# Optimization experiments

Measured on AMD Instinct MI355X. Metric: run time of the kernel, lower is better.

## Reference

```python
import jax, jax.numpy as jnp
import numpy as np

N, T, SAMPLES, OUT = 128, 1024, 1024, 8
TWO_PI = 2.0 * np.pi


def setup_inputs() -> dict:
    key = jax.random.key(0)
    ks = jax.random.split(key, 7)
    inp = jax.random.normal(ks[0], (N, T, 3), dtype=jnp.float32)
    h1, h2 = SAMPLES // 2, SAMPLES // 8
    W1 = jax.random.normal(ks[1], (h1, SAMPLES), dtype=jnp.float32) / np.sqrt(SAMPLES)
    b1 = jax.random.normal(ks[2], (h1,), dtype=jnp.float32) * 0.01
    W2 = jax.random.normal(ks[3], (h2, h1), dtype=jnp.float32) / np.sqrt(h1)
    b2 = jax.random.normal(ks[4], (h2,), dtype=jnp.float32) * 0.01
    W3 = jax.random.normal(ks[5], (OUT, h2), dtype=jnp.float32) / np.sqrt(h2)
    b3 = jax.random.normal(ks[6], (OUT,), dtype=jnp.float32) * 0.01
    return {"inp": inp, "W1": W1, "b1": b1, "W2": W2, "b2": b2, "W3": W3, "b3": b3}


def reference(inp, W1, b1, W2, b2, W3, b3):
    samples = W1.shape[1]
    t_len = inp.shape[1]
    x = inp[:, :, 0]          # [N, T] real signal
    day = inp[:, :, 2]        # [N, T] non-uniform times
    freqs = jnp.linspace(0.0, float(t_len - 1), samples, dtype=jnp.float32)
    # phase[n, s, t] = -2*pi * f_s * day[n, t]
    phase = (-TWO_PI) * freqs[None, :, None] * day[:, None, :]
    # complex exp split into real/imag panes; bmm fourier @ x -> [N, S]
    re = jnp.einsum('nst,nt->ns', jnp.cos(phase), x)
    im = jnp.einsum('nst,nt->ns', jnp.sin(phase), x)
    frequential = jnp.sqrt(re * re + im * im)  # |F x|, [N, samples]
    # 3-layer MLP with sigmoid activations (dropout = identity in eval)
    h = jax.nn.sigmoid(frequential @ W1.T + b1)
    h = jax.nn.sigmoid(h @ W2.T + b2)
    return h @ W3.T + b3
```

## Files before the change

kernel.cpp:

```cpp
#include <hip/hip_runtime.h>
#include <math.h>


#define NN   128
#define TT   1024
#define SS   1024
#define H1D  512
#define H2D  128
#define OUTD 8
#define KQN  8

#define MR    2048
#define WHALF 5
#define ALPHA 0.3702402f
#define BETA  6.35556e-6f
#define DSCALE 0.3432943f

#define OFF_SUBT 0
#define OFF_P1   (NN*512*4*2)

__device__ __forceinline__ float cos_rev(float r) { return __builtin_amdgcn_cosf(r); }
__device__ __forceinline__ float sin_rev(float r) { return __builtin_amdgcn_sinf(r); }

__device__ __forceinline__ float wave_sum(float v) {
#pragma unroll
    for (int off = 32; off > 0; off >>= 1) v += __shfl_xor(v, off, 64);
    return v;
}

__global__ __launch_bounds__(256) void k_sf(const float* __restrict__ inp,
                                            float* __restrict__ ws) {
    const int r   = blockIdx.x;
    const int n   = blockIdx.y;
    const int tid = threadIdx.x;

    __shared__ float2 Ag[512];
    __shared__ float2 Bg[512];

    Ag[tid] = make_float2(0.f, 0.f);
    Ag[tid + 256] = make_float2(0.f, 0.f);
    __syncthreads();

    const float* row = inp + (size_t)n * TT * 3;
#pragma unroll
    for (int pp = 0; pp < 4; ++pp) {
        const int t = pp * 256 + tid;
        const float x  = row[t * 3 + 0];
        const float d  = row[t * 3 + 2];
        const float df = d - floorf(d);
        const float p512 = 512.0f * df;
        const float r512 = p512 - floorf(p512);
        const float cre = x * cos_rev(r512);
        const float cim = -x * sin_rev(r512);
        const float z  = df * 2048.0f;
        const int   j0 = (int)z;
        const float dl = z - (float)j0;
        const int k0 = (r + 5 - j0 + 2048) & 3;
#pragma unroll
        for (int i = 0; i < 3; ++i) {
            const int   k = k0 + 4 * i;
            const float u = dl - (float)(k - WHALF);
            const float w = __expf(-ALPHA * u * u);
            const int  gi = (j0 + k - WHALF) & (MR - 1);
            const int   q = gi >> 2;
            atomicAdd(&Ag[q].x, w * cre);
            atomicAdd(&Ag[q].y, w * cim);
        }
    }
    __syncthreads();

    float2* src = Ag;
    float2* dst = Bg;
#pragma unroll
    for (int s = 0; s < 9; ++s) {
        const int   m    = 1 << s;
        const float invl = 1.0f / (float)(512 >> s);
        const int tau = tid;
        const int j   = tau >> s;
        const float rr = (float)j * invl;
        const float cv = cos_rev(rr), sv = sin_rev(rr);
        const float2 a = src[tau];
        const float2 b = src[tau + 256];
        const int o = tau + (tau & ~(m - 1));
        dst[o] = make_float2(a.x + b.x, a.y + b.y);
        const float dr = a.x - b.x, di = a.y - b.y;
        dst[o + m] = make_float2(fmaf(di, sv, dr * cv),
                                 fmaf(di, cv, -dr * sv));
        __syncthreads();
        float2* tmp = src; src = dst; dst = tmp;
    }

    float2* SUBT = (float2*)(ws + OFF_SUBT);
    SUBT[((size_t)n * 512 + tid)       * 4 + r] = src[tid];
    SUBT[((size_t)n * 512 + tid + 256) * 4 + r] = src[tid + 256];
}

__global__ __launch_bounds__(256) void k_cl1p(const float* __restrict__ W1,
                                              float* __restrict__ ws) {
    const int kq = blockIdx.x;
    const int jq = blockIdx.y;
    const int nb = blockIdx.z;
    const int tid = threadIdx.x;

    __shared__ float4 Al[8][32];
    float* Alf = (float*)Al;
    const float2* SUBT = (const float2*)(ws + OFF_SUBT);
#pragma unroll
    for (int i = 0; i < 4; ++i) {
        const int e    = i * 256 + tid;
        const int rown = e >> 7;
        const int kk   = e & 127;
        const int n    = nb * 8 + rown;
        const int ss   = kq * 128 + kk;
        const int k    = (ss + 1536) & (MR - 1);
        const int km   = ss & 511;
        const float2* F = SUBT + ((size_t)n * 512 + km) * 4;
        float2 X = F[0];
        const float f1 = (float)k * (1.0f / 2048.0f);
#pragma unroll
        for (int rr = 1; rr < 4; ++rr) {
            const float2 Fr = F[rr];
            const float fr = (float)rr * f1;
            const float ff = fr - floorf(fr);
            const float cv = cos_rev(ff), sv = sin_rev(ff);
            X.x = fmaf(Fr.x, cv, fmaf(Fr.y, sv, X.x));
            X.y = fmaf(Fr.y, cv, fmaf(-Fr.x, sv, X.y));
        }
        const int sp = ss - 512;
        const float D = DSCALE * __expf(BETA * (float)(sp * sp));
        Alf[e] = sqrtf(fmaf(X.x, X.x, X.y * X.y)) * D;
    }
    __syncthreads();

    const int jl = tid & 127, ng = tid >> 7;
    const int j = jq * 128 + jl;
    const float4* W1v = (const float4*)W1;
    float a0 = 0.f, a1 = 0.f, a2 = 0.f, a3 = 0.f;
#pragma unroll 4
    for (int k4 = 0; k4 < 32; ++k4) {
        const float4 w  = W1v[(size_t)j * 256 + kq * 32 + k4];
        const float4 x0 = Al[ng * 4 + 0][k4];
        const float4 x1 = Al[ng * 4 + 1][k4];
        const float4 x2 = Al[ng * 4 + 2][k4];
        const float4 x3 = Al[ng * 4 + 3][k4];
        a0 = fmaf(x0.x, w.x, fmaf(x0.y, w.y, fmaf(x0.z, w.z, fmaf(x0.w, w.w, a0))));
        a1 = fmaf(x1.x, w.x, fmaf(x1.y, w.y, fmaf(x1.z, w.z, fmaf(x1.w, w.w, a1))));
        a2 = fmaf(x2.x, w.x, fmaf(x2.y, w.y, fmaf(x2.z, w.z, fmaf(x2.w, w.w, a2))));
        a3 = fmaf(x3.x, w.x, fmaf(x3.y, w.y, fmaf(x3.z, w.z, fmaf(x3.w, w.w, a3))));
    }
    float* P1 = ws + OFF_P1;
    const float acc[4] = {a0, a1, a2, a3};
#pragma unroll
    for (int i = 0; i < 4; ++i)
        P1[((size_t)(kq * NN + nb * 8 + ng * 4 + i)) * H1D + j] = acc[i];
}

__global__ __launch_bounds__(1024) void k_mlp(const float* __restrict__ b1,
                                              const float* __restrict__ W2,
                                              const float* __restrict__ b2,
                                              const float* __restrict__ W3,
                                              const float* __restrict__ b3,
                                              const float* __restrict__ ws,
                                              float* __restrict__ out) {
    const int n   = blockIdx.x;
    const int tid = threadIdx.x;
    const int wid = tid >> 6, lane = tid & 63;

    __shared__ float h1L[H1D];
    __shared__ float h2L[H2D];

    if (tid < H1D) {
        const int j = tid;
        float s = b1[j];
#pragma unroll
        for (int kq = 0; kq < KQN; ++kq)
            s += ws[OFF_P1 + ((size_t)kq * NN + n) * H1D + j];
        h1L[j] = 1.0f / (1.0f + __expf(-s));
    }
    __syncthreads();

    {
        const float4* H1v = (const float4*)h1L;
        const float4 ha = H1v[lane], hb = H1v[64 + lane];
#pragma unroll
        for (int q = 0; q < 8; ++q) {
            const int j = wid * 8 + q;
            const float4* W2v = (const float4*)W2 + (size_t)j * 128;
            const float4 wa = W2v[lane], wb = W2v[64 + lane];
            float a = fmaf(wa.x, ha.x, fmaf(wa.y, ha.y, fmaf(wa.z, ha.z, wa.w * ha.w)));
            a = fmaf(wb.x, hb.x, fmaf(wb.y, hb.y, fmaf(wb.z, hb.z, fmaf(wb.w, hb.w, a))));
            a = wave_sum(a);
            if (lane == 0) h2L[j] = 1.0f / (1.0f + __expf(-(a + b2[j])));
        }
    }
    __syncthreads();

    if (wid < OUTD) {
        const float2 w = ((const float2*)W3)[wid * 64 + lane];
        const float2 h = ((const float2*)h2L)[lane];
        float a = fmaf(w.x, h.x, w.y * h.y);
        a = wave_sum(a);
        if (lane == 0) out[n * OUTD + wid] = a + b3[wid];
    }
}

extern "C" void kernel_launch(void* const* d_in, const int* in_sizes, int n_in,
                              void* d_out, int out_size, void* d_ws, size_t ws_size,
                              hipStream_t stream) {
    (void)in_sizes; (void)n_in; (void)out_size; (void)ws_size;
    const float* inp = (const float*)d_in[0];
    const float* W1  = (const float*)d_in[1];
    const float* b1  = (const float*)d_in[2];
    const float* W2  = (const float*)d_in[3];
    const float* b2  = (const float*)d_in[4];
    const float* W3  = (const float*)d_in[5];
    const float* b3  = (const float*)d_in[6];
    float* out = (float*)d_out;
    float* ws  = (float*)d_ws;

    k_sf  <<<dim3(4, NN),    dim3(256),  0, stream>>>(inp, ws);
    k_cl1p<<<dim3(8, 4, 16), dim3(256),  0, stream>>>(W1, ws);
    k_mlp <<<dim3(NN),       dim3(1024), 0, stream>>>(b1, W2, b2, W3, b3, ws, out);
}
```

Before: 43.02 us.

## Transpose W1 inside the spectrum kernel and remap layer-1 GEMV for coalesced loads

Measured after the change: 43.84 us. Within noise of the previous version (+1.9%).

```diff
diff --git a/kernel.cpp b/kernel.cpp
--- a/kernel.cpp
+++ b/kernel.cpp
@@ -1,6 +1,5 @@
 #include <hip/hip_runtime.h>
 #include <math.h>
-
 
 #define NN   128
 #define TT   1024
@@ -18,6 +17,7 @@
 
 #define OFF_SUBT 0
 #define OFF_P1   (NN*512*4*2)
+#define OFF_W1T  (OFF_P1 + KQN*NN*H1D)
 
 __device__ __forceinline__ float cos_rev(float r) { return __builtin_amdgcn_cosf(r); }
 __device__ __forceinline__ float sin_rev(float r) { return __builtin_amdgcn_sinf(r); }
@@ -29,6 +29,7 @@
 }
 
 __global__ __launch_bounds__(256) void k_sf(const float* __restrict__ inp,
+                                            const float* __restrict__ W1,
                                             float* __restrict__ ws) {
     const int r   = blockIdx.x;
     const int n   = blockIdx.y;
@@ -36,17 +37,36 @@
 
     __shared__ float2 Ag[512];
     __shared__ float2 Bg[512];
+    __shared__ float  tile[32][33];
 
     Ag[tid] = make_float2(0.f, 0.f);
     Ag[tid + 256] = make_float2(0.f, 0.f);
-    __syncthreads();
-
-    const float* row = inp + (size_t)n * TT * 3;
+
+    const int b  = r * NN + n;
+    const int jt = b & 15;
+    const int kt = b >> 4;
+    const int tc = tid & 31, tp = tid >> 5;
+#pragma unroll
+    for (int pass = 0; pass < 4; ++pass) {
+        const int row = pass * 8 + tp;
+        tile[row][tc] = W1[(size_t)(jt * 32 + row) * 1024 + kt * 32 + tc];
+    }
+    __syncthreads();
+    {
+        float* W1T = ws + OFF_W1T;
+#pragma unroll
+        for (int pass = 0; pass < 4; ++pass) {
+            const int row = pass * 8 + tp;
+            W1T[(size_t)(kt * 32 + row) * 512 + jt * 32 + tc] = tile[tc][row];
+        }
+    }
+
+    const float* row_ = inp + (size_t)n * TT * 3;
 #pragma unroll
     for (int pp = 0; pp < 4; ++pp) {
         const int t = pp * 256 + tid;
-        const float x  = row[t * 3 + 0];
-        const float d  = row[t * 3 + 2];
+        const float x  = row_[t * 3 + 0];
+        const float d  = row_[t * 3 + 2];
         const float df = d - floorf(d);
         const float p512 = 512.0f * df;
         const float r512 = p512 - floorf(p512);
@@ -80,10 +100,10 @@
         const float rr = (float)j * invl;
         const float cv = cos_rev(rr), sv = sin_rev(rr);
         const float2 a = src[tau];
-        const float2 b = src[tau + 256];
+        const float2 bb = src[tau + 256];
         const int o = tau + (tau & ~(m - 1));
-        dst[o] = make_float2(a.x + b.x, a.y + b.y);
-        const float dr = a.x - b.x, di = a.y - b.y;
+        dst[o] = make_float2(a.x + bb.x, a.y + bb.y);
+        const float dr = a.x - bb.x, di = a.y - bb.y;
         dst[o + m] = make_float2(fmaf(di, sv, dr * cv),
                                  fmaf(di, cv, -dr * sv));
         __syncthreads();
@@ -95,8 +115,7 @@
     SUBT[((size_t)n * 512 + tid + 256) * 4 + r] = src[tid + 256];
 }
 
-__global__ __launch_bounds__(256) void k_cl1p(const float* __restrict__ W1,
-                                              float* __restrict__ ws) {
+__global__ __launch_bounds__(256) void k_cl1p(float* __restrict__ ws) {
     const int kq = blockIdx.x;
     const int jq = blockIdx.y;
     const int nb = blockIdx.z;
@@ -132,27 +151,23 @@
     }
     __syncthreads();
 
-    const int jl = tid & 127, ng = tid >> 7;
-    const int j = jq * 128 + jl;
-    const float4* W1v = (const float4*)W1;
-    float a0 = 0.f, a1 = 0.f, a2 = 0.f, a3 = 0.f;
-#pragma unroll 4
-    for (int k4 = 0; k4 < 32; ++k4) {
-        const float4 w  = W1v[(size_t)j * 256 + kq * 32 + k4];
-        const float4 x0 = Al[ng * 4 + 0][k4];
-        const float4 x1 = Al[ng * 4 + 1][k4];
-        const float4 x2 = Al[ng * 4 + 2][k4];
-        const float4 x3 = Al[ng * 4 + 3][k4];
-        a0 = fmaf(x0.x, w.x, fmaf(x0.y, w.y, fmaf(x0.z, w.z, fmaf(x0.w, w.w, a0))));
-        a1 = fmaf(x1.x, w.x, fmaf(x1.y, w.y, fmaf(x1.z, w.z, fmaf(x1.w, w.w, a1))));
-        a2 = fmaf(x2.x, w.x, fmaf(x2.y, w.y, fmaf(x2.z, w.z, fmaf(x2.w, w.w, a2))));
-        a3 = fmaf(x3.x, w.x, fmaf(x3.y, w.y, fmaf(x3.z, w.z, fmaf(x3.w, w.w, a3))));
-    }
-    float* P1 = ws + OFF_P1;
-    const float acc[4] = {a0, a1, a2, a3};
-#pragma unroll
-    for (int i = 0; i < 4; ++i)
-        P1[((size_t)(kq * NN + nb * 8 + ng * 4 + i)) * H1D + j] = acc[i];
+    const int jv = tid & 31;
+    const int nh = tid >> 5;
+    const float4* W1T4 = (const float4*)(ws + OFF_W1T);
+    const float*  fqn  = Alf + nh * 128;
+    float4 acc = make_float4(0.f, 0.f, 0.f, 0.f);
+#pragma unroll 8
+    for (int k = 0; k < 128; ++k) {
+        const float4 w4 = W1T4[(size_t)(kq * 128 + k) * 128 + jq * 32 + jv];
+        const float  f  = fqn[k];
+        acc.x = fmaf(w4.x, f, acc.x);
+        acc.y = fmaf(w4.y, f, acc.y);
+        acc.z = fmaf(w4.z, f, acc.z);
+        acc.w = fmaf(w4.w, f, acc.w);
+    }
+    float4* P1v = (float4*)(ws + OFF_P1 +
+                            ((size_t)(kq * NN + nb * 8 + nh)) * H1D + jq * 128);
+    P1v[jv] = acc;
 }
 
 __global__ __launch_bounds__(1024) void k_mlp(const float* __restrict__ b1,
@@ -218,7 +233,7 @@
     float* out = (float*)d_out;
     float* ws  = (float*)d_ws;
 
-    k_sf  <<<dim3(4, NN),    dim3(256),  0, stream>>>(inp, ws);
-    k_cl1p<<<dim3(8, 4, 16), dim3(256),  0, stream>>>(W1, ws);
+    k_sf  <<<dim3(4, NN),    dim3(256),  0, stream>>>(inp, W1, ws);
+    k_cl1p<<<dim3(8, 4, 16), dim3(256),  0, stream>>>(ws);
     k_mlp <<<dim3(NN),       dim3(1024), 0, stream>>>(b1, W2, b2, W3, b3, ws, out);
 }
```
